# Performance work log

Hardware: AMD Instinct MI355X
Metric: run time of the kernel (lower is better)

## Reference

```python
import jax, jax.numpy as jnp
import numpy as np

B, S, D, H, E = 4, 2048, 512, 8, 4  # batch, seq, embed, heads, expand
HD = D // H


def setup_inputs() -> dict:
    key = jax.random.key(0)
    ks = jax.random.split(key, 9)
    s = lambda k, shape, fan: jax.random.normal(k, shape, jnp.float32) * (fan ** -0.5)
    return {
        "x": jax.random.normal(ks[0], (B, S, D), jnp.float32),
        "Wq": s(ks[1], (D, D), D),
        "Wk": s(ks[2], (D, D), D),
        "Wv": s(ks[3], (D, D), D),
        "Wo": s(ks[4], (D, D), D),
        "W1": s(ks[5], (D, D * E), D),
        "b1": jnp.zeros((D * E,), jnp.float32),
        "W2": s(ks[6], (D * E, D), D * E),
        "b2": jnp.zeros((D,), jnp.float32),
    }


def _encoder_layer(x, Wq, Wk, Wv, Wo, W1, b1, W2, b2):
    # NOTE: source computes InstanceNorm1d twice but discards both results -> no-ops.
    scale = D ** -0.25  # applied to BOTH q and k (net 1/sqrt(embed_dim))
    q = (x @ Wq).reshape(B, S, H, HD).transpose(0, 2, 1, 3) * scale  # [B,H,S,hd]
    k = (x @ Wk).reshape(B, S, H, HD).transpose(0, 2, 1, 3) * scale
    v = (x @ Wv).reshape(B, S, H, HD).transpose(0, 2, 1, 3)
    scores = jnp.einsum('bhqd,bhkd->bhqk', q, k)  # [B,H,S,S]
    attn = jax.nn.softmax(scores, axis=-1)
    o = jnp.einsum('bhqk,bhkd->bhqd', attn, v)  # [B,H,S,hd]
    o = o.transpose(0, 2, 1, 3).reshape(B, S, D)
    x = o @ Wo + x  # residual 1
    h = jax.nn.gelu(x @ W1 + b1, approximate=True)  # torch GELU(approximate='tanh')
    return h @ W2 + b2 + x  # residual 2 (dropout=0, eval)


def reference(x, Wq, Wk, Wv, Wo, W1, b1, W2, b2):
    return _encoder_layer(x, Wq, Wk, Wv, Wo, W1, b1, W2, b2)
```

## Files before the change

### kernel.cpp

```cpp
#include <hip/hip_runtime.h>
#include <hip/hip_bf16.h>


typedef __bf16 bf16;
typedef __attribute__((ext_vector_type(8))) __bf16 bf16x8;
typedef __attribute__((ext_vector_type(4))) __bf16 bf16x4;
typedef __attribute__((ext_vector_type(4))) float f32x4;
typedef __attribute__((ext_vector_type(16))) float f32x16;
typedef __attribute__((ext_vector_type(2))) unsigned int u32x2;
typedef __attribute__((ext_vector_type(4))) unsigned int u32x4;

#define LOG2E 1.4426950408889634f
#define SCORE_SCALE 0.044194173824159216f
#define SCALE_L2E (SCORE_SCALE * LOG2E)

#if __has_builtin(__builtin_amdgcn_exp2f)
#define EXP2(x) __builtin_amdgcn_exp2f(x)
#else
#define EXP2(x) exp2f(x)
#endif

__device__ __forceinline__ void gl_lds16(const bf16* g, bf16* l) {
  __builtin_amdgcn_global_load_lds(
      (const __attribute__((address_space(1))) unsigned int*)g,
      (__attribute__((address_space(3))) unsigned int*)l, 16, 0, 0);
}

template <int N>
__device__ __forceinline__ void wait_vm_barrier() {
  if constexpr (N == 0)
    asm volatile("s_waitcnt vmcnt(0)\ns_barrier" ::: "memory");
  else if constexpr (N == 3)
    asm volatile("s_waitcnt vmcnt(3)\ns_barrier" ::: "memory");
  else if constexpr (N == 4)
    asm volatile("s_waitcnt vmcnt(4)\ns_barrier" ::: "memory");
  else if constexpr (N == 8)
    asm volatile("s_waitcnt vmcnt(8)\ns_barrier" ::: "memory");
}

__device__ __forceinline__ float gelu_tanh(float x) {
  float u = 0.7978845608028654f * (x + 0.044715f * x * x * x);
  float e = EXP2(u * (2.0f * LOG2E));
  float th = 1.0f - 2.0f / (e + 1.0f);
  return 0.5f * x * (1.0f + th);
}

__device__ __forceinline__ f32x4 mfma_bf16(bf16x8 a, bf16x8 b, f32x4 c) {
  return __builtin_amdgcn_mfma_f32_16x16x32_bf16(a, b, c, 0, 0, 0);
}
__device__ __forceinline__ f32x16 mfma32x16(bf16x8 a, bf16x8 b, f32x16 c) {
  return __builtin_amdgcn_mfma_f32_32x32x16_bf16(a, b, c, 0, 0, 0);
}

__device__ __forceinline__ void plswap(unsigned int& a, unsigned int& b) {
  asm volatile("v_permlane32_swap_b32 %0, %1" : "+v"(a), "+v"(b));
}

__device__ __forceinline__ void xcd_remap(int& bx, int& by) {
  const int gx = gridDim.x;
  const int nwg = gx * gridDim.y;
  const int lin = blockIdx.y * gx + blockIdx.x;
  const int id = (lin & 7) * (nwg >> 3) + (lin >> 3);
  bx = id % gx;
  by = id / gx;
}

template <int MODE, typename OutT, int TN>
__global__ __launch_bounds__(256, 2) void gemm_bt(
    const bf16* __restrict__ A, const bf16* __restrict__ Bt,
    OutT* __restrict__ C, const float* __restrict__ bias,
    const float* __restrict__ resf, const bf16* __restrict__ resb,
    bf16* __restrict__ vt, int M, int N, int K) {
  constexpr int MI = (TN == 128) ? 4 : 2;
  constexpr int NBUF = (TN == 128) ? 2 : 3;
  __shared__ __align__(16) bf16 sA[NBUF][128 * 32];
  __shared__ __align__(16) bf16 sB[NBUF][TN * 32];
  const int tid = threadIdx.x;
  const int lane = tid & 63;
  const int quad = lane >> 4, lc = lane & 15;
  const int wave = tid >> 6;
  const int wr = (TN == 128) ? (wave >> 1) : wave;
  const int wc = (TN == 128) ? (wave & 1) : 0;
  int bxs, bys;
  xcd_remap(bxs, bys);
  const int m0 = bys * 128, n0 = bxs * TN;

  const int srow = tid >> 2;
  const int kc = (tid & 3) * 8;
  const bf16* Ag1 = A + (size_t)(m0 + srow) * K + kc;
  const bf16* Ag2 = A + (size_t)(m0 + 64 + srow) * K + kc;
  const bf16* Bg1 = Bt + (size_t)(n0 + srow) * K + kc;
  const bf16* Bg2 = Bt + (size_t)(n0 + 64 + srow) * K + kc;
  const int o1 = tid * 8, o2 = (tid + 256) * 8;

  f32x4 acc[MI][4];
#pragma unroll
  for (int mi = 0; mi < MI; ++mi)
#pragma unroll
    for (int ni = 0; ni < 4; ++ni) acc[mi][ni] = (f32x4){0.f, 0.f, 0.f, 0.f};

  const int kIters = K >> 5;

  if constexpr (TN == 128) {
    gl_lds16(Ag1, sA[0] + o1);
    gl_lds16(Ag2, sA[0] + o2);
    gl_lds16(Bg1, sB[0] + o1);
    gl_lds16(Bg2, sB[0] + o2);
    Ag1 += 32; Ag2 += 32; Bg1 += 32; Bg2 += 32;

    for (int kt = 0; kt < kIters; ++kt) {
      __syncthreads();
      const bf16* cA = sA[kt & 1];
      const bf16* cB = sB[kt & 1];
      if (kt + 1 < kIters) {
        bf16* nA = sA[(kt + 1) & 1];
        bf16* nB = sB[(kt + 1) & 1];
        gl_lds16(Ag1, nA + o1);
        gl_lds16(Ag2, nA + o2);
        gl_lds16(Bg1, nB + o1);
        gl_lds16(Bg2, nB + o2);
        Ag1 += 32; Ag2 += 32; Bg1 += 32; Bg2 += 32;
      }
      bf16x8 af[MI], bfm[4];
#pragma unroll
      for (int i = 0; i < MI; ++i)
        af[i] = *(const bf16x8*)(cA +
                                 ((wr * 64 + i * 16 + lc) * 32 + quad * 8));
#pragma unroll
      for (int i = 0; i < 4; ++i)
        bfm[i] =
            *(const bf16x8*)(cB + ((wc * 64 + i * 16 + lc) * 32 + quad * 8));
#pragma unroll
      for (int mi = 0; mi < MI; ++mi)
#pragma unroll
        for (int ni = 0; ni < 4; ++ni)
          acc[mi][ni] = mfma_bf16(af[mi], bfm[ni], acc[mi][ni]);
    }
  } else {
    auto stage = [&](int t) {
      bf16* a = sA[t % 3];
      bf16* bb = sB[t % 3];
      gl_lds16(Ag1 + t * 32, a + o1);
      gl_lds16(Ag2 + t * 32, a + o2);
      gl_lds16(Bg1 + t * 32, bb + o1);
    };
    stage(0);
    stage(1);
    for (int kt = 0; kt < kIters; ++kt) {
      if (kt + 1 < kIters)
        wait_vm_barrier<3>();
      else
        wait_vm_barrier<0>();
      if (kt + 2 < kIters) stage(kt + 2);
      const bf16* cA = sA[kt % 3];
      const bf16* cB = sB[kt % 3];
      bf16x8 af[MI], bfm[4];
#pragma unroll
      for (int i = 0; i < MI; ++i)
        af[i] = *(const bf16x8*)(cA +
                                 ((wr * 32 + i * 16 + lc) * 32 + quad * 8));
#pragma unroll
      for (int i = 0; i < 4; ++i)
        bfm[i] = *(const bf16x8*)(cB + ((i * 16 + lc) * 32 + quad * 8));
#pragma unroll
      for (int mi = 0; mi < MI; ++mi)
#pragma unroll
        for (int ni = 0; ni < 4; ++ni)
          acc[mi][ni] = mfma_bf16(af[mi], bfm[ni], acc[mi][ni]);
    }
  }

  if constexpr (MODE == 0) {
    if (n0 >= 1024) {
#pragma unroll
      for (int mi = 0; mi < MI; ++mi) {
        const int row0 = m0 + wr * (16 * MI) + mi * 16 + quad * 4;
        const int bb = row0 >> 11, s0 = row0 & 2047;
#pragma unroll
        for (int ni = 0; ni < 4; ++ni) {
          const int col = n0 + wc * 64 + ni * 16 + lc;
          const int hh = (col >> 6) & 7, d = col & 63;
          bf16x4 pb;
#pragma unroll
          for (int r = 0; r < 4; ++r) pb[r] = (bf16)acc[mi][ni][r];
          *(bf16x4*)(vt + ((size_t)((bb * 8 + hh) * 64 + d)) * 2048 + s0) = pb;
        }
      }
      return;
    }
  }
  const float qscale = (MODE == 0 && n0 < 512) ? SCALE_L2E : 1.0f;
#pragma unroll
  for (int mi = 0; mi < MI; ++mi) {
#pragma unroll
    for (int r = 0; r < 4; ++r) {
      const int row = m0 + wr * (16 * MI) + mi * 16 + quad * 4 + r;
#pragma unroll
      for (int ni = 0; ni < 4; ++ni) {
        const int col = n0 + wc * 64 + ni * 16 + lc;
        const size_t idx = (size_t)row * N + col;
        float v = acc[mi][ni][r];
        if (MODE == 0) v *= qscale;
        if (MODE == 1) v += resf[idx];
        if (MODE == 2) v = gelu_tanh(v + bias[col]);
        if (MODE == 3) v += bias[col] + (float)resb[idx];
        C[idx] = (OutT)v;
      }
    }
  }
}

__global__ __launch_bounds__(512, 2) void gemm256v2(
    const bf16* __restrict__ A, const bf16* __restrict__ Bt,
    bf16* __restrict__ C, const float* __restrict__ bias, int M, int N,
    int K) {
  __shared__ __align__(16) bf16 sA[4][8192];
  __shared__ __align__(16) bf16 sB[4][8192];
  const int tid = threadIdx.x;
  const int lane = tid & 63;
  const int quad = lane >> 4, lc = lane & 15;
  const int w8 = tid >> 6;
  const int wm = w8 >> 2, wn = w8 & 3;
  int bxs, bys;
  xcd_remap(bxs, bys);
  const int m0 = bys * 256, n0 = bxs * 256;

  const int srow0 = tid >> 2;
  const int cpos = tid & 3;

  f32x4 acc[8][4];
#pragma unroll
  for (int mi = 0; mi < 8; ++mi)
#pragma unroll
    for (int ni = 0; ni < 4; ++ni) acc[mi][ni] = (f32x4){0.f, 0.f, 0.f, 0.f};

  auto stage = [&](int t) {
    bf16* a = sA[t & 3];
    bf16* bb = sB[t & 3];
    const int k0 = t * 32;
#pragma unroll
    for (int c = 0; c < 2; ++c) {
      const int row = c * 128 + srow0;
      const int sc = (cpos ^ (row & 3)) * 8;
      gl_lds16(A + (size_t)(m0 + row) * K + k0 + sc, a + c * 4096 + tid * 8);
      gl_lds16(Bt + (size_t)(n0 + row) * K + k0 + sc, bb + c * 4096 + tid * 8);
    }
  };

  const int kIters = K >> 5;
  stage(0);
  stage(1);
  stage(2);

  const int cxq = (quad ^ (lc & 3)) << 3;

  for (int kt = 0; kt < kIters; ++kt) {
    const int left = kIters - 1 - kt;
    if (left >= 2)
      wait_vm_barrier<8>();
    else if (left == 1)
      wait_vm_barrier<4>();
    else
      wait_vm_barrier<0>();
    if (kt + 3 < kIters) stage(kt + 3);
    const bf16* cA = sA[kt & 3];
    const bf16* cB = sB[kt & 3];

    bf16x8 af[8], bfm[4];
#pragma unroll
    for (int i = 0; i < 4; ++i)
      af[i] = *(const bf16x8*)(cA + (wm * 128 + i * 16 + lc) * 32 + cxq);
#pragma unroll
    for (int j = 0; j < 4; ++j)
      bfm[j] = *(const bf16x8*)(cB + (wn * 64 + j * 16 + lc) * 32 + cxq);
    __builtin_amdgcn_s_barrier();
    __builtin_amdgcn_s_setprio(1);
#pragma unroll
    for (int mi = 0; mi < 4; ++mi)
#pragma unroll
      for (int ni = 0; ni < 4; ++ni)
        acc[mi][ni] = mfma_bf16(af[mi], bfm[ni], acc[mi][ni]);
    __builtin_amdgcn_s_setprio(0);
#pragma unroll
    for (int i = 4; i < 8; ++i)
      af[i] = *(const bf16x8*)(cA + (wm * 128 + i * 16 + lc) * 32 + cxq);
    __builtin_amdgcn_s_barrier();
    __builtin_amdgcn_s_setprio(1);
#pragma unroll
    for (int mi = 4; mi < 8; ++mi)
#pragma unroll
      for (int ni = 0; ni < 4; ++ni)
        acc[mi][ni] = mfma_bf16(af[mi], bfm[ni], acc[mi][ni]);
    __builtin_amdgcn_s_setprio(0);
  }

#pragma unroll
  for (int mi = 0; mi < 8; ++mi) {
#pragma unroll
    for (int r = 0; r < 4; ++r) {
      const int row = m0 + wm * 128 + mi * 16 + quad * 4 + r;
#pragma unroll
      for (int ni = 0; ni < 4; ++ni) {
        const int col = n0 + wn * 64 + ni * 16 + lc;
        C[(size_t)row * N + col] = (bf16)gelu_tanh(acc[mi][ni][r] + bias[col]);
      }
    }
  }
}

__global__ __launch_bounds__(256, 2) void flash_attn(
    const bf16* __restrict__ QKV, const bf16* __restrict__ Vt,
    bf16* __restrict__ O) {
  const int tid = threadIdx.x;
  const int lane = tid & 63, wave = tid >> 6;
  const int lo5 = lane & 31, hi = lane >> 5;
  const int lin = blockIdx.y * 16 + blockIdx.x;
  const int xcd = lin & 7, slot = lin >> 3;
  const int bh = xcd * 4 + (slot >> 4);
  const int qt = slot & 15;
  const int b = bh >> 3, h = bh & 7;
  const int q0 = qt * 128 + wave * 32;

  __shared__ __align__(16) bf16 sK[3][4096];
  __shared__ __align__(16) bf16 sV[3][4096];

  const bf16* Qrow = QKV + (size_t)(b * 2048 + q0 + lo5) * 1536 + h * 64;
  bf16x8 qf[4];
#pragma unroll
  for (int i = 0; i < 4; ++i) qf[i] = *(const bf16x8*)(Qrow + i * 16 + hi * 8);

  const int colsw = (((lane & 7) ^ (lane >> 3)) << 3);
  const bf16* Kg0 = QKV + (size_t)b * 2048 * 1536 + 512 + (size_t)h * 64 +
                    (size_t)(wave * 16 + (lane >> 3)) * 1536 + colsw;
  const bf16* Vg0 = Vt + (size_t)bh * 64 * 2048 +
                    (size_t)(wave * 16 + (lane >> 3)) * 2048 + colsw;
  const int stag = wave * 1024;
  const int m7 = lo5 & 7;

  f32x16 oacc[2];
  oacc[0] = (f32x16)(0.f);
  oacc[1] = (f32x16)(0.f);
  float rs0 = 0.f, rs1 = 0.f, rs2 = 0.f, rs3 = 0.f;

  auto stage = [&](int t) {
    bf16* dk = sK[t % 3] + stag;
    bf16* dv = sV[t % 3] + stag;
    gl_lds16(Kg0 + (size_t)t * 64 * 1536, dk);
    gl_lds16(Kg0 + (size_t)(t * 64 + 8) * 1536, dk + 512);
    gl_lds16(Vg0 + t * 64, dv);
    gl_lds16(Vg0 + t * 64 + 8 * 2048, dv + 512);
  };
  stage(0);
  stage(1);

  bf16x8 paw[4];

  auto softmax = [&](const f32x16& st, int hl) {
    unsigned int q32[4][2];
#pragma unroll
    for (int g = 0; g < 4; ++g) {
      bf16x4 pb;
      float p0 = EXP2(st[4 * g + 0]);
      float p1 = EXP2(st[4 * g + 1]);
      float p2 = EXP2(st[4 * g + 2]);
      float p3 = EXP2(st[4 * g + 3]);
      rs0 += p0; rs1 += p1; rs2 += p2; rs3 += p3;
      pb[0] = (bf16)p0; pb[1] = (bf16)p1; pb[2] = (bf16)p2; pb[3] = (bf16)p3;
      u32x2 w2 = __builtin_bit_cast(u32x2, pb);
      q32[g][0] = w2[0];
      q32[g][1] = w2[1];
    }
#pragma unroll
    for (int t = 0; t < 2; ++t) {
      unsigned int a0 = q32[2 * t][0], a1 = q32[2 * t][1];
      unsigned int b0 = q32[2 * t + 1][0], b1 = q32[2 * t + 1][1];
      plswap(a0, b0);
      plswap(a1, b1);
      u32x4 f = {a0, a1, b0, b1};
      paw[hl * 2 + t] = __builtin_bit_cast(bf16x8, f);
    }
  };

  for (int kt = 0; kt < 32; ++kt) {
    if (kt == 31)
      wait_vm_barrier<0>();
    else
      wait_vm_barrier<4>();
    if (kt + 2 < 32) stage(kt + 2);
    const bf16* cK = sK[kt % 3];
    const bf16* cV = sV[kt % 3];

    bf16x8 vf[2][4], kf[2][4];
#pragma unroll
    for (int dh = 0; dh < 2; ++dh) {
      const int Rd = dh * 32 + lo5;
#pragma unroll
      for (int w = 0; w < 4; ++w)
        vf[dh][w] =
            *(const bf16x8*)(cV + Rd * 64 + (((2 * w + hi) ^ m7) << 3));
    }
#pragma unroll
    for (int hl = 0; hl < 2; ++hl) {
      const int R = hl * 32 + lo5;
#pragma unroll
      for (int i = 0; i < 4; ++i)
        kf[hl][i] =
            *(const bf16x8*)(cK + R * 64 + (((2 * i + hi) ^ m7) << 3));
    }

    f32x16 st0 = (f32x16)(0.f), st1 = (f32x16)(0.f);
    __builtin_amdgcn_s_setprio(1);
#pragma unroll
    for (int i = 0; i < 4; ++i) {
      st0 = mfma32x16(kf[0][i], qf[i], st0);
      st1 = mfma32x16(kf[1][i], qf[i], st1);
    }
    __builtin_amdgcn_s_setprio(0);

    softmax(st0, 0);
#pragma unroll
    for (int w = 0; w < 2; ++w) {
      oacc[0] = mfma32x16(paw[w], vf[0][w], oacc[0]);
      oacc[1] = mfma32x16(paw[w], vf[1][w], oacc[1]);
    }
    softmax(st1, 1);
    __builtin_amdgcn_s_setprio(1);
#pragma unroll
    for (int w = 2; w < 4; ++w) {
      oacc[0] = mfma32x16(paw[w], vf[0][w], oacc[0]);
      oacc[1] = mfma32x16(paw[w], vf[1][w], oacc[1]);
    }
    __builtin_amdgcn_s_setprio(0);
  }

  float rsum = (rs0 + rs1) + (rs2 + rs3);
  rsum += __shfl_xor(rsum, 32, 64);
  const size_t obase = (size_t)(b * 2048 + q0) * 512 + h * 64;
#pragma unroll
  for (int r = 0; r < 16; ++r) {
    const int qloc = (r & 3) + 8 * (r >> 2) + 4 * hi;
    const float inv = 1.0f / __shfl(rsum, qloc, 64);
#pragma unroll
    for (int dh = 0; dh < 2; ++dh)
      O[obase + (size_t)qloc * 512 + dh * 32 + lo5] =
          (bf16)(oacc[dh][r] * inv);
  }
}

__global__ __launch_bounds__(256) void prep(
    const float* __restrict__ x, const float* __restrict__ Wq,
    const float* __restrict__ Wk, const float* __restrict__ Wv,
    const float* __restrict__ Wo, const float* __restrict__ W1,
    const float* __restrict__ W2, bf16* __restrict__ xb,
    bf16* __restrict__ WqkvT, bf16* __restrict__ WoT, bf16* __restrict__ W1T,
    bf16* __restrict__ W2T) {
  const int bid = blockIdx.x;
  if (bid < 4096) {
    const size_t i = ((size_t)bid * 256 + threadIdx.x) * 4;
    const float4 v = *(const float4*)(x + i);
    bf16x4 o;
    o[0] = (bf16)v.x; o[1] = (bf16)v.y; o[2] = (bf16)v.z; o[3] = (bf16)v.w;
    *(bf16x4*)(xb + i) = o;
    return;
  }
  const int t = bid - 4096;
  const float* in;
  bf16* out;
  int in_ld, out_ld, bx, by;
  if (t < 1024) {
    const int q = t >> 8, r = t & 255;
    bx = r & 15; by = r >> 4; in_ld = 512; out_ld = 512;
    in = (q == 0) ? Wq : (q == 1) ? Wk : (q == 2) ? Wv : Wo;
    out = (q == 0) ? WqkvT
          : (q == 1) ? WqkvT + 512 * 512
          : (q == 2) ? WqkvT + 2 * 512 * 512
                     : WoT;
  } else if (t < 2048) {
    const int r = t - 1024;
    bx = r & 63; by = r >> 6; in_ld = 2048; out_ld = 512;
    in = W1; out = W1T;
  } else {
    const int r = t - 2048;
    bx = r & 15; by = r >> 4; in_ld = 512; out_ld = 2048;
    in = W2; out = W2T;
  }
  __shared__ __align__(16) bf16 tl[32][33];
  const int tx = threadIdx.x & 31, ty = threadIdx.x >> 5;
  const int n0 = bx * 32, k0 = by * 32;
#pragma unroll
  for (int i = 0; i < 4; ++i)
    tl[ty + 8 * i][tx] = (bf16)in[(size_t)(k0 + ty + 8 * i) * in_ld + n0 + tx];
  __syncthreads();
#pragma unroll
  for (int i = 0; i < 4; ++i)
    out[(size_t)(n0 + ty + 8 * i) * out_ld + k0 + tx] = tl[tx][ty + 8 * i];
}

extern "C" void kernel_launch(void* const* d_in, const int* in_sizes, int n_in,
                              void* d_out, int out_size, void* d_ws,
                              size_t ws_size, hipStream_t stream) {
  const float* x = (const float*)d_in[0];
  const float* Wq = (const float*)d_in[1];
  const float* Wk = (const float*)d_in[2];
  const float* Wv = (const float*)d_in[3];
  const float* Wo = (const float*)d_in[4];
  const float* W1 = (const float*)d_in[5];
  const float* b1 = (const float*)d_in[6];
  const float* W2 = (const float*)d_in[7];
  const float* b2 = (const float*)d_in[8];
  float* out = (float*)d_out;

  char* ws = (char*)d_ws;
  size_t off = 0;
  auto alloc = [&](size_t bytes) {
    char* p = ws + off;
    off += (bytes + 255) & ~(size_t)255;
    return p;
  };
  bf16* WqkvT = (bf16*)alloc(1536ULL * 512 * 2);
  bf16* WoT = (bf16*)alloc(512ULL * 512 * 2);
  bf16* W1T = (bf16*)alloc(2048ULL * 512 * 2);
  bf16* W2T = (bf16*)alloc(512ULL * 2048 * 2);
  bf16* xb = (bf16*)alloc(8192ULL * 512 * 2);
  bf16* QKV = (bf16*)alloc(8192ULL * 1536 * 2);
  bf16* Vt = (bf16*)alloc(32ULL * 64 * 2048 * 2);
  bf16* attn = (bf16*)alloc(8192ULL * 512 * 2);
  bf16* x2 = xb;
  bf16* hbuf = QKV;

  const dim3 tb(256);
  prep<<<dim3(7168), tb, 0, stream>>>(x, Wq, Wk, Wv, Wo, W1, W2, xb, WqkvT,
                                      WoT, W1T, W2T);
  gemm_bt<0, bf16, 128><<<dim3(12, 64), tb, 0, stream>>>(
      xb, WqkvT, QKV, nullptr, nullptr, nullptr, Vt, 8192, 1536, 512);
  flash_attn<<<dim3(16, 32), tb, 0, stream>>>(QKV, Vt, attn);
  gemm_bt<1, bf16, 64><<<dim3(8, 64), tb, 0, stream>>>(
      attn, WoT, x2, nullptr, x, nullptr, nullptr, 8192, 512, 512);
  gemm256v2<<<dim3(8, 32), dim3(512), 0, stream>>>(x2, W1T, hbuf, b1, 8192,
                                                   2048, 512);
  gemm_bt<3, float, 64><<<dim3(8, 64), tb, 0, stream>>>(
      hbuf, W2T, out, b2, nullptr, x2, nullptr, 8192, 512, 2048);
}
```

Baseline: 239.0 us.

## Split flash attention over two key halves and combine partial sums

The attention kernel now splits the key/value range into two halves along a new grid dimension, doubling the block count. Each half writes unnormalized fp32 partial outputs and row sums, and a new combine kernel adds them and normalizes into bf16. The V buffer drops to double buffering, with a reworked prefetch schedule and occupancy hint raised to 4 blocks per CU. This is meant to fill more of the GPU during attention. In exchange it adds fp32 partial-output traffic and an extra kernel launch. Skipping the max subtraction stays valid because the halves share a common exponent base.

Measured after the change: 285.0 us. 1.19x slower.

```diff
diff --git a/kernel.cpp b/kernel.cpp
--- a/kernel.cpp
+++ b/kernel.cpp
@@ -30,6 +30,8 @@
 __device__ __forceinline__ void wait_vm_barrier() {
   if constexpr (N == 0)
     asm volatile("s_waitcnt vmcnt(0)\ns_barrier" ::: "memory");
+  else if constexpr (N == 2)
+    asm volatile("s_waitcnt vmcnt(2)\ns_barrier" ::: "memory");
   else if constexpr (N == 3)
     asm volatile("s_waitcnt vmcnt(3)\ns_barrier" ::: "memory");
   else if constexpr (N == 4)
@@ -308,9 +310,9 @@
   }
 }
 
-__global__ __launch_bounds__(256, 2) void flash_attn(
+__global__ __launch_bounds__(256, 4) void flash_attn(
     const bf16* __restrict__ QKV, const bf16* __restrict__ Vt,
-    bf16* __restrict__ O) {
+    float* __restrict__ O0, float* __restrict__ O1, float* __restrict__ Rp) {
   const int tid = threadIdx.x;
   const int lane = tid & 63, wave = tid >> 6;
   const int lo5 = lane & 31, hi = lane >> 5;
@@ -320,9 +322,11 @@
   const int qt = slot & 15;
   const int b = bh >> 3, h = bh & 7;
   const int q0 = qt * 128 + wave * 32;
+  const int half = blockIdx.z;
+  const int t0 = half << 4;
 
   __shared__ __align__(16) bf16 sK[3][4096];
-  __shared__ __align__(16) bf16 sV[3][4096];
+  __shared__ __align__(16) bf16 sV[2][4096];
 
   const bf16* Qrow = QKV + (size_t)(b * 2048 + q0 + lo5) * 1536 + h * 64;
   bf16x8 qf[4];
@@ -342,16 +346,21 @@
   oacc[1] = (f32x16)(0.f);
   float rs0 = 0.f, rs1 = 0.f, rs2 = 0.f, rs3 = 0.f;
 
-  auto stage = [&](int t) {
-    bf16* dk = sK[t % 3] + stag;
-    bf16* dv = sV[t % 3] + stag;
-    gl_lds16(Kg0 + (size_t)t * 64 * 1536, dk);
-    gl_lds16(Kg0 + (size_t)(t * 64 + 8) * 1536, dk + 512);
-    gl_lds16(Vg0 + t * 64, dv);
-    gl_lds16(Vg0 + t * 64 + 8 * 2048, dv + 512);
+  auto stageK = [&](int lt) {
+    bf16* dk = sK[lt % 3] + stag;
+    const int g = t0 + lt;
+    gl_lds16(Kg0 + (size_t)g * 64 * 1536, dk);
+    gl_lds16(Kg0 + (size_t)(g * 64 + 8) * 1536, dk + 512);
   };
-  stage(0);
-  stage(1);
+  auto stageV = [&](int lt) {
+    bf16* dv = sV[lt & 1] + stag;
+    const int g = t0 + lt;
+    gl_lds16(Vg0 + g * 64, dv);
+    gl_lds16(Vg0 + g * 64 + 8 * 2048, dv + 512);
+  };
+  stageK(0);
+  stageV(0);
+  stageK(1);
 
   bf16x8 paw[4];
 
@@ -381,14 +390,15 @@
     }
   };
 
-  for (int kt = 0; kt < 32; ++kt) {
-    if (kt == 31)
+  for (int kt = 0; kt < 16; ++kt) {
+    if (kt == 15)
       wait_vm_barrier<0>();
     else
-      wait_vm_barrier<4>();
-    if (kt + 2 < 32) stage(kt + 2);
+      wait_vm_barrier<2>();
+    if (kt + 1 < 16) stageV(kt + 1);
+    if (kt + 2 < 16) stageK(kt + 2);
     const bf16* cK = sK[kt % 3];
-    const bf16* cV = sV[kt % 3];
+    const bf16* cV = sV[kt & 1];
 
     bf16x8 vf[2][4], kf[2][4];
 #pragma unroll
@@ -435,16 +445,36 @@
 
   float rsum = (rs0 + rs1) + (rs2 + rs3);
   rsum += __shfl_xor(rsum, 32, 64);
+  float* Op = half ? O1 : O0;
   const size_t obase = (size_t)(b * 2048 + q0) * 512 + h * 64;
 #pragma unroll
   for (int r = 0; r < 16; ++r) {
     const int qloc = (r & 3) + 8 * (r >> 2) + 4 * hi;
-    const float inv = 1.0f / __shfl(rsum, qloc, 64);
 #pragma unroll
     for (int dh = 0; dh < 2; ++dh)
-      O[obase + (size_t)qloc * 512 + dh * 32 + lo5] =
-          (bf16)(oacc[dh][r] * inv);
-  }
+      Op[obase + (size_t)qloc * 512 + dh * 32 + lo5] = oacc[dh][r];
+  }
+  if (hi == 0)
+    Rp[(size_t)(half * 8 + h) * 8192 + b * 2048 + q0 + lo5] = rsum;
+}
+
+__global__ __launch_bounds__(256) void combine(
+    const float* __restrict__ O0, const float* __restrict__ O1,
+    const float* __restrict__ Rp, bf16* __restrict__ attn) {
+  const int i4 = blockIdx.x * 256 + threadIdx.x;
+  const int row = i4 >> 7;
+  const int col = (i4 & 127) * 4;
+  const int h = col >> 6;
+  const float inv =
+      1.0f / (Rp[(size_t)h * 8192 + row] + Rp[(size_t)(8 + h) * 8192 + row]);
+  const float4 a = ((const float4*)O0)[i4];
+  const float4 b = ((const float4*)O1)[i4];
+  bf16x4 o;
+  o[0] = (bf16)((a.x + b.x) * inv);
+  o[1] = (bf16)((a.y + b.y) * inv);
+  o[2] = (bf16)((a.z + b.z) * inv);
+  o[3] = (bf16)((a.w + b.w) * inv);
+  *(bf16x4*)(attn + (size_t)i4 * 4) = o;
 }
 
 __global__ __launch_bounds__(256) void prep(
@@ -525,6 +555,9 @@
   bf16* QKV = (bf16*)alloc(8192ULL * 1536 * 2);
   bf16* Vt = (bf16*)alloc(32ULL * 64 * 2048 * 2);
   bf16* attn = (bf16*)alloc(8192ULL * 512 * 2);
+  float* Opart1 = (float*)alloc(8192ULL * 512 * 4);
+  float* Rpart = (float*)alloc(2ULL * 8 * 8192 * 4);
+  float* Opart0 = out;
   bf16* x2 = xb;
   bf16* hbuf = QKV;
 
@@ -533,7 +566,9 @@
                                       WoT, W1T, W2T);
   gemm_bt<0, bf16, 128><<<dim3(12, 64), tb, 0, stream>>>(
       xb, WqkvT, QKV, nullptr, nullptr, nullptr, Vt, 8192, 1536, 512);
-  flash_attn<<<dim3(16, 32), tb, 0, stream>>>(QKV, Vt, attn);
+  flash_attn<<<dim3(16, 32, 2), tb, 0, stream>>>(QKV, Vt, Opart0, Opart1,
+                                                 Rpart);
+  combine<<<dim3(4096), tb, 0, stream>>>(Opart0, Opart1, Rpart, attn);
   gemm_bt<1, bf16, 64><<<dim3(8, 64), tb, 0, stream>>>(
       attn, WoT, x2, nullptr, x, nullptr, nullptr, 8192, 512, 512);
   gemm256v2<<<dim3(8, 32), dim3(512), 0, stream>>>(x2, W1T, hbuf, b1, 8192,
```
